# Kernel optimization log

Measured on AMD Instinct MI355X. Metric: run time of the kernel, lower is better.

The kernel has to match this reference:

```python
import jax, jax.numpy as jnp
import numpy as np

TOKENS, D_MODEL, VOCAB = 4096, 2048, 32000

def setup_inputs() -> dict:
    key = jax.random.key(0)
    k1, k2, k3 = jax.random.split(key, 3)
    x = jax.random.normal(k1, (TOKENS, D_MODEL), dtype=jnp.float32)
    w = jax.random.normal(k2, (VOCAB, D_MODEL), dtype=jnp.float32) * 0.02
    target = jax.random.randint(k3, (TOKENS,), 0, VOCAB, dtype=jnp.int64)
    return {"x": x, "w": w, "target": target}

def reference(x, w, target):
    # Fused fc + log_softmax + NLL (sum reduction), scale=None so LMCL is off.
    # logits: [tokens, vocab]
    logits = jnp.einsum('td,vd->tv', x, w)
    m = jnp.max(logits, axis=-1)                      # online-max equivalent
    s = jnp.sum(jnp.exp(logits - m[:, None]), axis=-1)  # debased exp-sums
    tgt_score = jnp.take_along_axis(logits, target[:, None], axis=1)[:, 0]
    # prob = exp(tgt - m) / s ; loss = -sum(log(prob)) = -(tgt - m - log(s)).sum()
    log_prob = tgt_score - m - jnp.log(s)
    return -jnp.sum(log_prob)
```

## Files before the change

### kernel.cpp

```cpp
#include <hip/hip_runtime.h>
#include <hip/hip_bf16.h>
#include <math.h>

#define TOKENS 4096
#define DMODEL 2048
#define VOCAB  32000

#define BM2 256
#define BK2 32
#define NKT 64
#define MT  16
#define NT  125

#define BM 128
#define BN 128
#define BK 64
#define NI 5
#define VSLICE (BN*NI)
#define VS (VOCAB/VSLICE)
#define KT (DMODEL/BK)

typedef __attribute__((ext_vector_type(8))) short bf16x8;
typedef __attribute__((ext_vector_type(4))) float f32x4;
typedef __attribute__((ext_vector_type(4))) unsigned int u32x4;

__device__ __forceinline__ unsigned int cvt_pk_bf16(float a, float b) {
  unsigned int r;
  asm volatile("v_cvt_pk_bf16_f32 %0, %1, %2" : "=v"(r) : "v"(a), "v"(b));
  return r;
}

__device__ __forceinline__ void gload16(const unsigned char* g, unsigned char* l) {
  __builtin_amdgcn_global_load_lds((const __attribute__((address_space(1))) unsigned int*)g,
                                   (__attribute__((address_space(3))) unsigned int*)l,
                                   16, 0, 0);
}

__global__ void init_kernel(float* __restrict__ s_acc, float* __restrict__ out) {
  int i = blockIdx.x * 256 + threadIdx.x;
  if (i < TOKENS) s_acc[i] = 0.0f;
  if (i == 0) *out = 0.0f;
}

__global__ void tgt_kernel(const float* __restrict__ x, const float* __restrict__ w,
                           const int* __restrict__ target, float* __restrict__ tgt_score) {
  int wid  = threadIdx.x >> 6;
  int lane = threadIdx.x & 63;
  int row  = blockIdx.x * 4 + wid;
  if (row >= TOKENS) return;
  int t = target[row];
  const float4* xr = (const float4*)(x + (size_t)row * DMODEL);
  const float4* wr = (const float4*)(w + (size_t)t   * DMODEL);
  float acc = 0.0f;
  #pragma unroll
  for (int i = 0; i < DMODEL/4/64; ++i) {
    float4 a = xr[lane + i*64];
    float4 b = wr[lane + i*64];
    acc += a.x*b.x + a.y*b.y + a.z*b.z + a.w*b.w;
  }
  #pragma unroll
  for (int d = 1; d < 64; d <<= 1) acc += __shfl_xor(acc, d);
  if (lane == 0) tgt_score[row] = acc;
}

__global__ void conv_kernel(const float* __restrict__ src,
                            unsigned char* __restrict__ hp,
                            unsigned char* __restrict__ lp) {
  size_t u = (size_t)blockIdx.x * 256 + threadIdx.x;
  size_t byteoff = u << 4;
  int chunk = (int)(byteoff >> 14);
  int o     = (int)(byteoff & 16383);
  int rb    = chunk >> 6;
  int kt    = chunk & 63;
  int row   = o >> 6;
  int colb  = (o & 63) ^ (((row >> 1) & 3) << 4);
  const float* s = src + (size_t)(rb * 256 + row) * DMODEL + kt * 32 + (colb >> 1);
  const float4 v0 = ((const float4*)s)[0];
  const float4 v1 = ((const float4*)s)[1];

  unsigned int h0 = cvt_pk_bf16(v0.x, v0.y);
  unsigned int h1 = cvt_pk_bf16(v0.z, v0.w);
  unsigned int h2 = cvt_pk_bf16(v1.x, v1.y);
  unsigned int h3 = cvt_pk_bf16(v1.z, v1.w);
  float r0 = v0.x - __uint_as_float(h0 << 16);
  float r1 = v0.y - __uint_as_float(h0 & 0xFFFF0000u);
  float r2 = v0.z - __uint_as_float(h1 << 16);
  float r3 = v0.w - __uint_as_float(h1 & 0xFFFF0000u);
  float r4 = v1.x - __uint_as_float(h2 << 16);
  float r5 = v1.y - __uint_as_float(h2 & 0xFFFF0000u);
  float r6 = v1.z - __uint_as_float(h3 << 16);
  float r7 = v1.w - __uint_as_float(h3 & 0xFFFF0000u);
  unsigned int l0 = cvt_pk_bf16(r0, r1);
  unsigned int l1 = cvt_pk_bf16(r2, r3);
  unsigned int l2 = cvt_pk_bf16(r4, r5);
  unsigned int l3 = cvt_pk_bf16(r6, r7);

  *(u32x4*)(hp + byteoff) = (u32x4){h0, h1, h2, h3};
  *(u32x4*)(lp + byteoff) = (u32x4){l0, l1, l2, l3};
}

template<int BUFR, int BUFW>
__device__ __forceinline__ void ktile(
    unsigned char* lds,
    const unsigned char* __restrict__ xh, const unsigned char* __restrict__ xl,
    const unsigned char* __restrict__ wh, const unsigned char* __restrict__ wl,
    size_t abase, size_t bbase, int ktn, int st0, int st1,
    int wr, int wc, int laneoff, f32x4 (&acc)[8][4])
{
  asm volatile("s_waitcnt vmcnt(0)" ::: "memory");
  __builtin_amdgcn_s_barrier();
  __builtin_amdgcn_sched_barrier(0);

  if (ktn < NKT) {
    const size_t ca = abase + ((size_t)ktn << 14);
    const size_t cb = bbase + ((size_t)ktn << 14);
    gload16(xh + ca + st0, lds + BUFW + st0);
    gload16(xh + ca + st1, lds + BUFW + st1);
    gload16(xl + ca + st0, lds + BUFW + 16384 + st0);
    gload16(xl + ca + st1, lds + BUFW + 16384 + st1);
    gload16(wh + cb + st0, lds + BUFW + 32768 + st0);
    gload16(wh + cb + st1, lds + BUFW + 32768 + st1);
    gload16(wl + cb + st0, lds + BUFW + 49152 + st0);
    gload16(wl + cb + st1, lds + BUFW + 49152 + st1);
  }
  __builtin_amdgcn_sched_barrier(0);

  bf16x8 bh[4], bl[4];
  #pragma unroll
  for (int n = 0; n < 4; ++n) {
    const int bo = BUFR + 32768 + wc * 4096 + n * 1024 + laneoff;
    bh[n] = *(const bf16x8*)(lds + bo);
    bl[n] = *(const bf16x8*)(lds + bo + 16384);
  }
  #pragma unroll
  for (int p = 0; p < 4; ++p) {
    bf16x8 ah[2], al[2];
    #pragma unroll
    for (int mm = 0; mm < 2; ++mm) {
      const int ao = BUFR + wr * 8192 + (p * 2 + mm) * 1024 + laneoff;
      ah[mm] = *(const bf16x8*)(lds + ao);
      al[mm] = *(const bf16x8*)(lds + ao + 16384);
    }
    __builtin_amdgcn_s_setprio(1);
    #pragma unroll
    for (int mm = 0; mm < 2; ++mm)
      #pragma unroll
      for (int n = 0; n < 4; ++n) {
        acc[p*2+mm][n] = __builtin_amdgcn_mfma_f32_16x16x32_bf16(ah[mm], bh[n], acc[p*2+mm][n], 0, 0, 0);
        acc[p*2+mm][n] = __builtin_amdgcn_mfma_f32_16x16x32_bf16(ah[mm], bl[n], acc[p*2+mm][n], 0, 0, 0);
        acc[p*2+mm][n] = __builtin_amdgcn_mfma_f32_16x16x32_bf16(al[mm], bh[n], acc[p*2+mm][n], 0, 0, 0);
      }
    __builtin_amdgcn_s_setprio(0);
  }
}

__global__ __launch_bounds__(512, 2)
void gemm_packed8(const unsigned char* __restrict__ xh, const unsigned char* __restrict__ xl,
                  const unsigned char* __restrict__ wh, const unsigned char* __restrict__ wl,
                  float* __restrict__ s_acc)
{
  __shared__ unsigned char lds[131072];

  const int tid  = threadIdx.x;
  const int lane = tid & 63;
  const int wid  = tid >> 6;
  const int wr   = wid >> 2;
  const int wc   = wid & 3;
  const int l15  = lane & 15;
  const int lq   = lane >> 4;

  const int wg    = blockIdx.x;
  const int swz   = (wg & 7) * 250 + (wg >> 3);
  const int vtile = swz >> 4;
  const int mtile = swz & 15;

  const size_t abase = ((size_t)(mtile * NKT)) << 14;
  const size_t bbase = ((size_t)(vtile * NKT)) << 14;
  const int st0 = tid << 4;
  const int st1 = 8192 + (tid << 4);
  const int laneoff = l15 * 64 + ((lq * 16) ^ (((l15 >> 1) & 3) << 4));

  f32x4 acc[8][4];
  #pragma unroll
  for (int m = 0; m < 8; ++m)
    #pragma unroll
    for (int n = 0; n < 4; ++n)
      acc[m][n] = (f32x4){0.f, 0.f, 0.f, 0.f};

  gload16(xh + abase + st0, lds + st0);
  gload16(xh + abase + st1, lds + st1);
  gload16(xl + abase + st0, lds + 16384 + st0);
  gload16(xl + abase + st1, lds + 16384 + st1);
  gload16(wh + bbase + st0, lds + 32768 + st0);
  gload16(wh + bbase + st1, lds + 32768 + st1);
  gload16(wl + bbase + st0, lds + 49152 + st0);
  gload16(wl + bbase + st1, lds + 49152 + st1);

  for (int t = 0; t < NKT; t += 2) {
    ktile<0, 65536>(lds, xh, xl, wh, wl, abase, bbase, t + 1, st0, st1, wr, wc, laneoff, acc);
    ktile<65536, 0>(lds, xh, xl, wh, wl, abase, bbase, t + 2, st0, st1, wr, wc, laneoff, acc);
  }
  asm volatile("s_waitcnt vmcnt(0)" ::: "memory");

  #pragma unroll
  for (int m = 0; m < 8; ++m) {
    #pragma unroll
    for (int j = 0; j < 4; ++j) {
      float e = 0.f;
      #pragma unroll
      for (int n = 0; n < 4; ++n) e += __expf(acc[m][n][j]);
      e += __shfl_xor(e, 1);
      e += __shfl_xor(e, 2);
      e += __shfl_xor(e, 4);
      e += __shfl_xor(e, 8);
      if (l15 == 0)
        atomicAdd(&s_acc[mtile * BM2 + wr * 128 + m * 16 + lq * 4 + j], e);
    }
  }
}

__global__ __launch_bounds__(256, 2)
void gemm_fallback(const float* __restrict__ x, const float* __restrict__ w,
                   float* __restrict__ s_acc) {
  __shared__ unsigned char lds[4 * BM * BK * 2];
  const int AH = 0, AL = 16384, BH = 32768, BL = 49152;
  const int tid  = threadIdx.x;
  const int lane = tid & 63;
  const int wid  = tid >> 6;
  const int wrr  = wid >> 1;
  const int wcc  = wid & 1;
  const int l15  = lane & 15;
  const int lq   = lane >> 4;
  const int mbase  = blockIdx.y * BM;
  const int nslice = blockIdx.x * VSLICE;

  float s_part[16];
  #pragma unroll
  for (int i = 0; i < 16; ++i) s_part[i] = 0.0f;

  for (int bn = 0; bn < NI; ++bn) {
    const int nbase = nslice + bn * BN;
    f32x4 acc[4][4];
    #pragma unroll
    for (int m = 0; m < 4; ++m)
      #pragma unroll
      for (int n = 0; n < 4; ++n)
        acc[m][n] = (f32x4){0.f, 0.f, 0.f, 0.f};

    for (int kt = 0; kt < KT; ++kt) {
      const int kb = kt * BK;
      __syncthreads();
      #pragma unroll
      for (int i = 0; i < 8; ++i) {
        const int T   = tid + (i & 3) * 256;
        const int row = T >> 3;
        const int kg  = T & 7;
        const float* src = (i < 4)
            ? (x + (size_t)(mbase + row) * DMODEL + kb + kg * 8)
            : (w + (size_t)(nbase + row) * DMODEL + kb + kg * 8);
        const float4 v0 = ((const float4*)src)[0];
        const float4 v1 = ((const float4*)src)[1];
        unsigned int h0 = cvt_pk_bf16(v0.x, v0.y);
        unsigned int h1 = cvt_pk_bf16(v0.z, v0.w);
        unsigned int h2 = cvt_pk_bf16(v1.x, v1.y);
        unsigned int h3 = cvt_pk_bf16(v1.z, v1.w);
        float r0 = v0.x - __uint_as_float(h0 << 16);
        float r1 = v0.y - __uint_as_float(h0 & 0xFFFF0000u);
        float r2 = v0.z - __uint_as_float(h1 << 16);
        float r3 = v0.w - __uint_as_float(h1 & 0xFFFF0000u);
        float r4 = v1.x - __uint_as_float(h2 << 16);
        float r5 = v1.y - __uint_as_float(h2 & 0xFFFF0000u);
        float r6 = v1.z - __uint_as_float(h3 << 16);
        float r7 = v1.w - __uint_as_float(h3 & 0xFFFF0000u);
        unsigned int l0 = cvt_pk_bf16(r0, r1);
        unsigned int l1 = cvt_pk_bf16(r2, r3);
        unsigned int l2 = cvt_pk_bf16(r4, r5);
        unsigned int l3 = cvt_pk_bf16(r6, r7);
        const int byteoff = row * 128 + ((kg * 16) ^ ((row & 7) << 4));
        const int hbase = (i < 4) ? AH : BH;
        const int lbase = (i < 4) ? AL : BL;
        *(u32x4*)(lds + hbase + byteoff) = (u32x4){h0, h1, h2, h3};
        *(u32x4*)(lds + lbase + byteoff) = (u32x4){l0, l1, l2, l3};
      }
      __syncthreads();

      #pragma unroll
      for (int kh = 0; kh < 2; ++kh) {
        bf16x8 ah[4], al[4];
        #pragma unroll
        for (int m = 0; m < 4; ++m) {
          const int row = wrr * 64 + m * 16 + l15;
          const int bo  = row * 128 + ((kh * 64 + lq * 16) ^ ((row & 7) << 4));
          ah[m] = *(const bf16x8*)(lds + AH + bo);
          al[m] = *(const bf16x8*)(lds + AL + bo);
        }
        #pragma unroll
        for (int n = 0; n < 4; ++n) {
          const int row = wcc * 64 + n * 16 + l15;
          const int bo  = row * 128 + ((kh * 64 + lq * 16) ^ ((row & 7) << 4));
          bf16x8 bh = *(const bf16x8*)(lds + BH + bo);
          bf16x8 bl = *(const bf16x8*)(lds + BL + bo);
          #pragma unroll
          for (int m = 0; m < 4; ++m) {
            acc[m][n] = __builtin_amdgcn_mfma_f32_16x16x32_bf16(ah[m], bh, acc[m][n], 0, 0, 0);
            acc[m][n] = __builtin_amdgcn_mfma_f32_16x16x32_bf16(ah[m], bl, acc[m][n], 0, 0, 0);
            acc[m][n] = __builtin_amdgcn_mfma_f32_16x16x32_bf16(al[m], bh, acc[m][n], 0, 0, 0);
          }
        }
      }
    }

    #pragma unroll
    for (int m = 0; m < 4; ++m)
      #pragma unroll
      for (int j = 0; j < 4; ++j) {
        float e = 0.0f;
        #pragma unroll
        for (int n = 0; n < 4; ++n) e += __expf(acc[m][n][j]);
        s_part[m * 4 + j] += e;
      }
  }

  #pragma unroll
  for (int i = 0; i < 16; ++i) {
    float vv = s_part[i];
    vv += __shfl_xor(vv, 1);
    vv += __shfl_xor(vv, 2);
    vv += __shfl_xor(vv, 4);
    vv += __shfl_xor(vv, 8);
    s_part[i] = vv;
  }
  if (l15 == 0) {
    #pragma unroll
    for (int m = 0; m < 4; ++m)
      #pragma unroll
      for (int j = 0; j < 4; ++j) {
        const int row = mbase + wrr * 64 + m * 16 + lq * 4 + j;
        atomicAdd(&s_acc[row], s_part[m * 4 + j]);
      }
  }
}

__global__ void loss_kernel(const float* __restrict__ s_acc,
                            const float* __restrict__ tgt_score,
                            float* __restrict__ out) {
  int i = blockIdx.x * 256 + threadIdx.x;
  float v = logf(s_acc[i]) - tgt_score[i];
  #pragma unroll
  for (int d = 1; d < 64; d <<= 1) v += __shfl_xor(v, d);
  if ((threadIdx.x & 63) == 0) atomicAdd(out, v);
}

extern "C" void kernel_launch(void* const* d_in, const int* in_sizes, int n_in,
                              void* d_out, int out_size, void* d_ws, size_t ws_size,
                              hipStream_t stream) {
  const float* x      = (const float*)d_in[0];
  const float* w      = (const float*)d_in[1];
  const int*   target = (const int*)d_in[2];
  float* out = (float*)d_out;

  float* s_acc     = (float*)d_ws;
  float* tgt_score = s_acc + TOKENS;
  unsigned char* base = (unsigned char*)(tgt_score + TOKENS);
  const size_t XPLANE = (size_t)TOKENS * DMODEL * 2;
  const size_t WPLANE = (size_t)VOCAB  * DMODEL * 2;
  unsigned char* xh = base;
  unsigned char* xl = xh + XPLANE;
  unsigned char* wh = xl + XPLANE;
  unsigned char* wl = wh + WPLANE;
  const size_t needed = (size_t)2 * TOKENS * 4 + 2 * XPLANE + 2 * WPLANE;

  init_kernel<<<(TOKENS + 255) / 256, 256, 0, stream>>>(s_acc, out);
  tgt_kernel<<<TOKENS / 4, 256, 0, stream>>>(x, w, target, tgt_score);

  if (ws_size >= needed) {
    conv_kernel<<<(int)(XPLANE / 16 / 256), 256, 0, stream>>>(x, xh, xl);
    conv_kernel<<<(int)(WPLANE / 16 / 256), 256, 0, stream>>>(w, wh, wl);
    gemm_packed8<<<MT * NT, 512, 0, stream>>>(xh, xl, wh, wl, s_acc);
  } else {
    gemm_fallback<<<dim3(VS, TOKENS / BM), 256, 0, stream>>>(x, w, s_acc);
  }

  loss_kernel<<<TOKENS / 256, 256, 0, stream>>>(s_acc, tgt_score, out);
}
```

Before: 1.495 ms.

## Replace split-bf16 three-MFMA GEMM with single bf16 pass

Removes the low-order bf16 residual planes for x and w, so the conversion writes only one bf16 plane and the GEMM issues one MFMA per product instead of three. LDS staging halves, and launch bounds are raised to allow more resident workgroups. This cuts matrix-core work and global/LDS traffic. The cost is that logits lose the extra precision the hi/lo split provided, which may affect the accuracy of the summed loss.

```diff
diff --git a/kernel.cpp b/kernel.cpp
--- a/kernel.cpp
+++ b/kernel.cpp
@@ -11,6 +11,7 @@
 #define NKT 64
 #define MT  16
 #define NT  125
+#define BUF1 32768
 
 #define BM 128
 #define BN 128
@@ -64,8 +65,7 @@
 }
 
 __global__ void conv_kernel(const float* __restrict__ src,
-                            unsigned char* __restrict__ hp,
-                            unsigned char* __restrict__ lp) {
+                            unsigned char* __restrict__ hp) {
   size_t u = (size_t)blockIdx.x * 256 + threadIdx.x;
   size_t byteoff = u << 4;
   int chunk = (int)(byteoff >> 14);
@@ -77,33 +77,17 @@
   const float* s = src + (size_t)(rb * 256 + row) * DMODEL + kt * 32 + (colb >> 1);
   const float4 v0 = ((const float4*)s)[0];
   const float4 v1 = ((const float4*)s)[1];
-
   unsigned int h0 = cvt_pk_bf16(v0.x, v0.y);
   unsigned int h1 = cvt_pk_bf16(v0.z, v0.w);
   unsigned int h2 = cvt_pk_bf16(v1.x, v1.y);
   unsigned int h3 = cvt_pk_bf16(v1.z, v1.w);
-  float r0 = v0.x - __uint_as_float(h0 << 16);
-  float r1 = v0.y - __uint_as_float(h0 & 0xFFFF0000u);
-  float r2 = v0.z - __uint_as_float(h1 << 16);
-  float r3 = v0.w - __uint_as_float(h1 & 0xFFFF0000u);
-  float r4 = v1.x - __uint_as_float(h2 << 16);
-  float r5 = v1.y - __uint_as_float(h2 & 0xFFFF0000u);
-  float r6 = v1.z - __uint_as_float(h3 << 16);
-  float r7 = v1.w - __uint_as_float(h3 & 0xFFFF0000u);
-  unsigned int l0 = cvt_pk_bf16(r0, r1);
-  unsigned int l1 = cvt_pk_bf16(r2, r3);
-  unsigned int l2 = cvt_pk_bf16(r4, r5);
-  unsigned int l3 = cvt_pk_bf16(r6, r7);
-
   *(u32x4*)(hp + byteoff) = (u32x4){h0, h1, h2, h3};
-  *(u32x4*)(lp + byteoff) = (u32x4){l0, l1, l2, l3};
 }
 
 template<int BUFR, int BUFW>
 __device__ __forceinline__ void ktile(
     unsigned char* lds,
-    const unsigned char* __restrict__ xh, const unsigned char* __restrict__ xl,
-    const unsigned char* __restrict__ wh, const unsigned char* __restrict__ wl,
+    const unsigned char* __restrict__ xh, const unsigned char* __restrict__ wh,
     size_t abase, size_t bbase, int ktn, int st0, int st1,
     int wr, int wc, int laneoff, f32x4 (&acc)[8][4])
 {
@@ -116,50 +100,38 @@
     const size_t cb = bbase + ((size_t)ktn << 14);
     gload16(xh + ca + st0, lds + BUFW + st0);
     gload16(xh + ca + st1, lds + BUFW + st1);
-    gload16(xl + ca + st0, lds + BUFW + 16384 + st0);
-    gload16(xl + ca + st1, lds + BUFW + 16384 + st1);
-    gload16(wh + cb + st0, lds + BUFW + 32768 + st0);
-    gload16(wh + cb + st1, lds + BUFW + 32768 + st1);
-    gload16(wl + cb + st0, lds + BUFW + 49152 + st0);
-    gload16(wl + cb + st1, lds + BUFW + 49152 + st1);
+    gload16(wh + cb + st0, lds + BUFW + 16384 + st0);
+    gload16(wh + cb + st1, lds + BUFW + 16384 + st1);
   }
   __builtin_amdgcn_sched_barrier(0);
 
-  bf16x8 bh[4], bl[4];
-  #pragma unroll
-  for (int n = 0; n < 4; ++n) {
-    const int bo = BUFR + 32768 + wc * 4096 + n * 1024 + laneoff;
-    bh[n] = *(const bf16x8*)(lds + bo);
-    bl[n] = *(const bf16x8*)(lds + bo + 16384);
-  }
-  #pragma unroll
-  for (int p = 0; p < 4; ++p) {
-    bf16x8 ah[2], al[2];
-    #pragma unroll
-    for (int mm = 0; mm < 2; ++mm) {
-      const int ao = BUFR + wr * 8192 + (p * 2 + mm) * 1024 + laneoff;
-      ah[mm] = *(const bf16x8*)(lds + ao);
-      al[mm] = *(const bf16x8*)(lds + ao + 16384);
-    }
+  bf16x8 bh[4];
+  #pragma unroll
+  for (int n = 0; n < 4; ++n)
+    bh[n] = *(const bf16x8*)(lds + BUFR + 16384 + wc * 4096 + n * 1024 + laneoff);
+
+  #pragma unroll
+  for (int p = 0; p < 2; ++p) {
+    bf16x8 ah[4];
+    #pragma unroll
+    for (int mm = 0; mm < 4; ++mm)
+      ah[mm] = *(const bf16x8*)(lds + BUFR + wr * 8192 + (p * 4 + mm) * 1024 + laneoff);
     __builtin_amdgcn_s_setprio(1);
     #pragma unroll
-    for (int mm = 0; mm < 2; ++mm)
-      #pragma unroll
-      for (int n = 0; n < 4; ++n) {
-        acc[p*2+mm][n] = __builtin_amdgcn_mfma_f32_16x16x32_bf16(ah[mm], bh[n], acc[p*2+mm][n], 0, 0, 0);
-        acc[p*2+mm][n] = __builtin_amdgcn_mfma_f32_16x16x32_bf16(ah[mm], bl[n], acc[p*2+mm][n], 0, 0, 0);
-        acc[p*2+mm][n] = __builtin_amdgcn_mfma_f32_16x16x32_bf16(al[mm], bh[n], acc[p*2+mm][n], 0, 0, 0);
-      }
+    for (int mm = 0; mm < 4; ++mm)
+      #pragma unroll
+      for (int n = 0; n < 4; ++n)
+        acc[p*4+mm][n] = __builtin_amdgcn_mfma_f32_16x16x32_bf16(ah[mm], bh[n], acc[p*4+mm][n], 0, 0, 0);
     __builtin_amdgcn_s_setprio(0);
   }
 }
 
-__global__ __launch_bounds__(512, 2)
-void gemm_packed8(const unsigned char* __restrict__ xh, const unsigned char* __restrict__ xl,
-                  const unsigned char* __restrict__ wh, const unsigned char* __restrict__ wl,
+__global__ __launch_bounds__(512, 4)
+void gemm_packed8(const unsigned char* __restrict__ xh,
+                  const unsigned char* __restrict__ wh,
                   float* __restrict__ s_acc)
 {
-  __shared__ unsigned char lds[131072];
+  __shared__ unsigned char lds[65536];
 
   const int tid  = threadIdx.x;
   const int lane = tid & 63;
@@ -189,16 +161,12 @@
 
   gload16(xh + abase + st0, lds + st0);
   gload16(xh + abase + st1, lds + st1);
-  gload16(xl + abase + st0, lds + 16384 + st0);
-  gload16(xl + abase + st1, lds + 16384 + st1);
-  gload16(wh + bbase + st0, lds + 32768 + st0);
-  gload16(wh + bbase + st1, lds + 32768 + st1);
-  gload16(wl + bbase + st0, lds + 49152 + st0);
-  gload16(wl + bbase + st1, lds + 49152 + st1);
+  gload16(wh + bbase + st0, lds + 16384 + st0);
+  gload16(wh + bbase + st1, lds + 16384 + st1);
 
   for (int t = 0; t < NKT; t += 2) {
-    ktile<0, 65536>(lds, xh, xl, wh, wl, abase, bbase, t + 1, st0, st1, wr, wc, laneoff, acc);
-    ktile<65536, 0>(lds, xh, xl, wh, wl, abase, bbase, t + 2, st0, st1, wr, wc, laneoff, acc);
+    ktile<0, BUF1>(lds, xh, wh, abase, bbase, t + 1, st0, st1, wr, wc, laneoff, acc);
+    ktile<BUF1, 0>(lds, xh, wh, abase, bbase, t + 2, st0, st1, wr, wc, laneoff, acc);
   }
   asm volatile("s_waitcnt vmcnt(0)" ::: "memory");
 
@@ -365,18 +333,16 @@
   const size_t XPLANE = (size_t)TOKENS * DMODEL * 2;
   const size_t WPLANE = (size_t)VOCAB  * DMODEL * 2;
   unsigned char* xh = base;
-  unsigned char* xl = xh + XPLANE;
-  unsigned char* wh = xl + XPLANE;
-  unsigned char* wl = wh + WPLANE;
-  const size_t needed = (size_t)2 * TOKENS * 4 + 2 * XPLANE + 2 * WPLANE;
+  unsigned char* wh = xh + XPLANE;
+  const size_t needed = (size_t)2 * TOKENS * 4 + XPLANE + WPLANE;
 
   init_kernel<<<(TOKENS + 255) / 256, 256, 0, stream>>>(s_acc, out);
   tgt_kernel<<<TOKENS / 4, 256, 0, stream>>>(x, w, target, tgt_score);
 
   if (ws_size >= needed) {
-    conv_kernel<<<(int)(XPLANE / 16 / 256), 256, 0, stream>>>(x, xh, xl);
-    conv_kernel<<<(int)(WPLANE / 16 / 256), 256, 0, stream>>>(w, wh, wl);
-    gemm_packed8<<<MT * NT, 512, 0, stream>>>(xh, xl, wh, wl, s_acc);
+    conv_kernel<<<(int)(XPLANE / 16 / 256), 256, 0, stream>>>(x, xh);
+    conv_kernel<<<(int)(WPLANE / 16 / 256), 256, 0, stream>>>(w, wh);
+    gemm_packed8<<<MT * NT, 512, 0, stream>>>(xh, wh, s_acc);
   } else {
     gemm_fallback<<<dim3(VS, TOKENS / BM), 256, 0, stream>>>(x, w, s_acc);
   }
```

New measurement: 4.769 ms. 3.19x slower.
